# Optimization experiments

Measured on AMD Instinct MI355X. Metric: run time of the kernel, lower is better.

Reference implementation:

```python
import jax, jax.numpy as jnp
import numpy as np

INF = jnp.float32(1e30)


def _lsap_square(cost):
    """Exact Jonker-Volgenant shortest-augmenting-path LAP (port of scipy's
    rectangular_lsap) on a square [n, n] float32 cost matrix.
    Returns col4row[int32, n]: column assigned to each row (a permutation)."""
    n = cost.shape[0]
    rows = jnp.arange(n, dtype=jnp.int32)

    def outer(cur_row, carry):
        u, v, col4row, row4col = carry

        def dij_cond(st):
            return st[6] < 0

        def dij_body(st):
            i, minVal, SR, SC, sp, path, sink = st
            SR = SR.at[i].set(True)
            # tentative shortest-path cost through row i to every column
            r = minVal + cost[i] - u[i] - v
            upd = (~SC) & (r < sp)
            path = jnp.where(upd, i, path)
            sp = jnp.where(upd, r, sp)
            masked = jnp.where(SC, INF, sp)
            j = jnp.argmin(masked).astype(jnp.int32)
            minVal = masked[j]
            SC = SC.at[j].set(True)
            nxt = row4col[j]
            sink = jnp.where(nxt < 0, j, jnp.int32(-1))
            i = jnp.where(nxt < 0, i, nxt)
            return (i, minVal, SR, SC, sp, path, sink)

        init = (cur_row.astype(jnp.int32), jnp.float32(0.0),
                jnp.zeros(n, bool), jnp.zeros(n, bool),
                jnp.full(n, INF, jnp.float32),
                jnp.full(n, -1, jnp.int32), jnp.int32(-1))
        _, minVal, SR, SC, sp, path, sink = jax.lax.while_loop(dij_cond, dij_body, init)

        # dual potential updates
        sp_c4r = sp[jnp.clip(col4row, 0, n - 1)]
        du = jnp.where(rows == cur_row, minVal, minVal - sp_c4r)
        u = u + jnp.where(SR, du, jnp.float32(0.0))
        v = v - jnp.where(SC, minVal - sp, jnp.float32(0.0))

        # augment along the alternating path ending at sink
        def aug_cond(st):
            return ~st[3]

        def aug_body(st):
            j, c4r, r4c, done = st
            i = path[j]
            r4c = r4c.at[j].set(i)
            jnew = c4r[i]
            c4r = c4r.at[i].set(j)
            done = (i == cur_row)
            return (jnew, c4r, r4c, done)

        _, col4row, row4col, _ = jax.lax.while_loop(
            aug_cond, aug_body, (sink, col4row, row4col, jnp.bool_(False)))
        return (u, v, col4row, row4col)

    z = jnp.zeros(n, jnp.float32)
    neg1 = jnp.full(n, -1, jnp.int32)
    _, _, col4row, _ = jax.lax.fori_loop(0, n, outer, (z, z, neg1, neg1))
    return col4row


def _match(costs, mask):
    # costs: [B, N, N] (dim1 = preds, dim2 = objects); mask: [B, N] prefix-valid objects
    B, N, _ = costs.shape
    cols = jnp.arange(N, dtype=jnp.int32)

    def one(cost_b, mask_b):
        # rows = objects, cols = preds (matches costs[k][:, :n].T in torch code);
        # invalid object rows get constant cost 0, which leaves the optimal
        # matching of valid rows unchanged.
        cmat = jnp.where(mask_b[:, None], cost_b.T, jnp.float32(0.0))
        col4row = _lsap_square(cmat)
        # columns consumed by valid rows
        used = jnp.zeros(N, bool).at[col4row].set(mask_b)
        # unused columns ascending first, then used columns ascending
        leftover = jnp.sort(cols + N * used.astype(jnp.int32)) % N
        n = jnp.sum(mask_b).astype(jnp.int32)
        pos = jnp.clip(cols - n, 0, N - 1)
        # valid rows: matched column; invalid rows: leftover preds in ascending order
        return jnp.where(mask_b, col4row, leftover[pos])

    return jax.vmap(one)(costs, mask)


def setup_inputs() -> dict:
    key = jax.random.key(0)
    k1, k2 = jax.random.split(key)
    B, N = 64, 256
    costs = jax.random.normal(k1, (B, N, N), dtype=jnp.float32)
    lengths = jax.random.randint(k2, (B,), N // 2, N + 1)
    object_valid_mask = jnp.arange(N)[None, :] < lengths[:, None]  # prefix-true mask
    return {"costs": costs, "object_valid_mask": object_valid_mask}


def reference(costs, object_valid_mask):
    return _match(costs.astype(jnp.float32), object_valid_mask)
```

## Files before the change

### kernel.cpp

```cpp
#include <hip/hip_runtime.h>

#define NN 256
#define INFV 1e30f

__device__ __forceinline__ int mask_fmt(const void* m) {
    int w0 = ((const int*)m)[0];
    if (w0 == 1) return 0;
    if (w0 == 0x3F800000) return 1;
    return 2;
}
__device__ __forceinline__ bool mask_at(const void* m, int fmt, int idx) {
    if (fmt == 0) return ((const int*)m)[idx] != 0;
    if (fmt == 1) return ((const float*)m)[idx] != 0.0f;
    return ((const unsigned char*)m)[idx] != 0;
}

__global__ void transpose_mask_kernel(const float* __restrict__ costs,
                                      const void* __restrict__ mask,
                                      float* __restrict__ ws) {
    __shared__ float tile[32][33];
    const int b  = blockIdx.z;
    const int i0 = blockIdx.x * 32;
    const int j0 = blockIdx.y * 32;
    const int tx = threadIdx.x;
    const int ty = threadIdx.y;
    const int fmt = mask_fmt(mask);
    const float* Cb = costs + (size_t)b * NN * NN;
    float* Wb = ws + (size_t)b * NN * NN;

    #pragma unroll
    for (int k = 0; k < 32; k += 8) {
        tile[ty + k][tx] = Cb[(size_t)(j0 + ty + k) * NN + (i0 + tx)];
    }
    __syncthreads();
    #pragma unroll
    for (int k = 0; k < 32; k += 8) {
        const int i = i0 + ty + k;
        const int j = j0 + tx;
        const bool mv = mask_at(mask, fmt, b * NN + i);
        Wb[(size_t)i * NN + j] = mv ? tile[tx][ty + k] : 0.0f;
    }
}

__device__ __forceinline__ int rl(int v, int lane) {
    return __builtin_amdgcn_readlane(v, lane);
}
__device__ __forceinline__ float rlf(float v, int lane) {
    return __int_as_float(__builtin_amdgcn_readlane(__float_as_int(v), lane));
}
__device__ __forceinline__ int read4i(const int a[4], int idx) {
    const int lane = idx >> 2;
    const int v0 = rl(a[0], lane), v1 = rl(a[1], lane);
    const int v2 = rl(a[2], lane), v3 = rl(a[3], lane);
    const int lo = (idx & 1) ? v1 : v0;
    const int hi = (idx & 1) ? v3 : v2;
    return (idx & 2) ? hi : lo;
}
__device__ __forceinline__ float read4f(const float a[4], int idx) {
    const int lane = idx >> 2;
    const int v0 = rl(__float_as_int(a[0]), lane), v1 = rl(__float_as_int(a[1]), lane);
    const int v2 = rl(__float_as_int(a[2]), lane), v3 = rl(__float_as_int(a[3]), lane);
    const int lo = (idx & 1) ? v1 : v0;
    const int hi = (idx & 1) ? v3 : v2;
    return __int_as_float((idx & 2) ? hi : lo);
}
__device__ __forceinline__ void write4i(int (&a)[4], int idx, int val, int lane) {
    if (lane == (idx >> 2)) {
        switch (idx & 3) {
            case 0: a[0] = val; break;
            case 1: a[1] = val; break;
            case 2: a[2] = val; break;
            default: a[3] = val; break;
        }
    }
}

template <int CTRL>
__device__ __forceinline__ float dpp_mov_f(float x) {
    return __int_as_float(__builtin_amdgcn_update_dpp(
        __float_as_int(x), __float_as_int(x), CTRL, 0xf, 0xf, false));
}
__device__ __forceinline__ float wave_min64(float x) {
    x = fminf(x, dpp_mov_f<0x111>(x));
    x = fminf(x, dpp_mov_f<0x112>(x));
    x = fminf(x, dpp_mov_f<0x114>(x));
    x = fminf(x, dpp_mov_f<0x118>(x));
    x = fminf(x, dpp_mov_f<0x142>(x));
    x = fminf(x, dpp_mov_f<0x143>(x));
    return rlf(x, 63);
}

template <bool USE_WS>
__global__ __launch_bounds__(64)
void lap_kernel(const float* __restrict__ costs,
                const void* __restrict__ mask,
                const float* __restrict__ cmat,
                int* __restrict__ out,
                int rcache) {
    extern __shared__ float ldsrows[];

    const int b    = blockIdx.x;
    const int lane = threadIdx.x;

    __shared__ float sp_s[NN];
    __shared__ int   tmp_s[NN];

    const int fmt = mask_fmt(mask);

    int nloc = 0;
    #pragma unroll
    for (int r = 0; r < 4; ++r)
        nloc += mask_at(mask, fmt, b * NN + lane * 4 + r) ? 1 : 0;
    #pragma unroll
    for (int off = 32; off; off >>= 1) nloc += __shfl_xor(nloc, off);
    const int n = nloc;

    float u[4]  = {0.f, 0.f, 0.f, 0.f};
    float v[4]  = {0.f, 0.f, 0.f, 0.f};
    int  c4r[4] = {-1, -1, -1, -1};
    int  r4c[4] = {-1, -1, -1, -1};

    const float* CM = cmat + (size_t)b * NN * NN;
    const float* CB = costs + (size_t)b * NN * NN;

    if (USE_WS) {
        #pragma unroll 4
        for (int row = 0; row < rcache; ++row) {
            const int base = row * NN + lane * 4;
            *reinterpret_cast<float4*>(&ldsrows[base]) =
                *reinterpret_cast<const float4*>(CM + base);
        }
        __syncthreads();
    }

    for (int cur = 0; cur < NN; ++cur) {
        float sp[4]  = {INFV, INFV, INFV, INFV};
        int  path[4] = {-1, -1, -1, -1};
        int   SCm = 0, SRm = 0;
        int   i      = cur;
        float minVal = 0.0f;
        int   sink   = -1;

        for (int guard = 0; guard <= NN && sink < 0; ++guard) {
            if (lane == (i >> 2)) SRm |= 1 << (i & 3);

            float cc[4];
            if (USE_WS) {
                if (i < rcache) {
                    const float4 c4 = *reinterpret_cast<const float4*>(&ldsrows[i * NN + lane * 4]);
                    cc[0] = c4.x; cc[1] = c4.y; cc[2] = c4.z; cc[3] = c4.w;
                } else {
                    const float4 c4 = *reinterpret_cast<const float4*>(CM + (size_t)i * NN + lane * 4);
                    cc[0] = c4.x; cc[1] = c4.y; cc[2] = c4.z; cc[3] = c4.w;
                }
            } else {
                if (i < n) {
                    #pragma unroll
                    for (int r = 0; r < 4; ++r)
                        cc[r] = CB[(size_t)(lane * 4 + r) * NN + i];
                } else {
                    #pragma unroll
                    for (int r = 0; r < 4; ++r) cc[r] = 0.0f;
                }
            }
            const float u_i = read4f(u, i);

            float m[4];
            #pragma unroll
            for (int r = 0; r < 4; ++r) {
                const float rr = minVal + cc[r] - u_i - v[r];
                const bool sc = (SCm >> r) & 1;
                if (!sc && rr < sp[r]) { sp[r] = rr; path[r] = i; }
                m[r] = sc ? INFV : sp[r];
            }

            minVal = wave_min64(fminf(fminf(m[0], m[1]), fminf(m[2], m[3])));

            int cand = 4;
            if (m[3] == minVal) cand = 3;
            if (m[2] == minVal) cand = 2;
            if (m[1] == minVal) cand = 1;
            if (m[0] == minVal) cand = 0;
            const unsigned long long bal = __ballot(cand < 4);
            const int fl = (bal == 0ull) ? 0 : (__ffsll((long long)bal) - 1);
            const int j  = (bal == 0ull) ? 0 : (fl * 4 + rl(cand, fl));

            if (lane == (j >> 2)) SCm |= 1 << (j & 3);
            const int nxt = read4i(r4c, j);
            if (nxt < 0) sink = j;
            else         i = nxt;
        }

        *reinterpret_cast<float4*>(&sp_s[lane * 4]) = make_float4(sp[0], sp[1], sp[2], sp[3]);
        __syncthreads();

        #pragma unroll
        for (int r = 0; r < 4; ++r) {
            const int row = lane * 4 + r;
            if ((SRm >> r) & 1) {
                float du;
                if (row == cur) {
                    du = minVal;
                } else {
                    int c = c4r[r];
                    c = c < 0 ? 0 : c;
                    du = minVal - sp_s[c];
                }
                u[r] = u[r] + du;
            }
            if ((SCm >> r) & 1) v[r] = v[r] - (minVal - sp[r]);
        }
        __syncthreads();

        {
            int j = sink;
            for (int guard = 0; guard < NN; ++guard) {
                const int ii = read4i(path, j);
                write4i(r4c, j, ii, lane);
                const int jn = read4i(c4r, ii);
                write4i(c4r, ii, j, lane);
                if (ii == cur) break;
                j = jn;
            }
        }
    }

    int* ob = out + b * NN;
    #pragma unroll
    for (int r = 0; r < 4; ++r) {
        const int row = lane * 4 + r;
        if (row < n) ob[row] = c4r[r];
        tmp_s[lane * 4 + r] = r4c[r];
    }
    __syncthreads();
    if (lane == 0) {
        int cnt = 0;
        for (int c = 0; c < NN; ++c) {
            if (tmp_s[c] >= n) {
                ob[n + cnt] = c;
                ++cnt;
            }
        }
    }
}

extern "C" void kernel_launch(void* const* d_in, const int* in_sizes, int n_in,
                              void* d_out, int out_size, void* d_ws, size_t ws_size,
                              hipStream_t stream) {
    const float* costs = (const float*)d_in[0];
    const void*  mask  = d_in[1];
    int*         out   = (int*)d_out;

    const int B = in_sizes[1] / NN;
    const size_t need = (size_t)B * NN * NN * sizeof(float);

    if (ws_size >= need && d_ws != nullptr) {
        float* ws = (float*)d_ws;
        transpose_mask_kernel<<<dim3(NN / 32, NN / 32, B), dim3(32, 8), 0, stream>>>(costs, mask, ws);

        int rcache = 158;
        hipError_t e = hipFuncSetAttribute(
            reinterpret_cast<const void*>(&lap_kernel<true>),
            hipFuncAttributeMaxDynamicSharedMemorySize,
            rcache * NN * (int)sizeof(float));
        if (e != hipSuccess) rcache = 60;
        const size_t dynbytes = (size_t)rcache * NN * sizeof(float);

        lap_kernel<true><<<dim3(B), dim3(64), dynbytes, stream>>>(costs, mask, ws, out, rcache);
    } else {
        lap_kernel<false><<<dim3(B), dim3(64), 0, stream>>>(costs, mask, nullptr, out, 0);
    }
}
```

Before: 5.676 ms.

## Precompute masked-min off critical path and prefetch next cost row in Dijkstra loop

Restructures the inner Dijkstra step so the wave-wide minimum over previously masked columns (Vprev) is computed after selecting j, and the current step only reduces the freshly computed row costs before combining with Vprev. Scanned columns are masked by adding INF through a scadd array instead of branching on the SC bitmask. The next row load is issued right after j is known, so its latency can overlap the trailing reduction. This adds a second wave reduction per iteration and relies on INF arithmetic to keep masked columns from winning, and changes ballot logic which must match tie-breaking exactly.

```diff
diff --git a/kernel.cpp b/kernel.cpp
--- a/kernel.cpp
+++ b/kernel.cpp
@@ -123,6 +123,27 @@
     const float* CM = cmat + (size_t)b * NN * NN;
     const float* CB = costs + (size_t)b * NN * NN;
 
+    auto load_row = [&](int irow, float (&cc)[4]) {
+        if (USE_WS) {
+            if (irow < rcache) {
+                const float4 c4 = *reinterpret_cast<const float4*>(&ldsrows[irow * NN + lane * 4]);
+                cc[0] = c4.x; cc[1] = c4.y; cc[2] = c4.z; cc[3] = c4.w;
+            } else {
+                const float4 c4 = *reinterpret_cast<const float4*>(CM + (size_t)irow * NN + lane * 4);
+                cc[0] = c4.x; cc[1] = c4.y; cc[2] = c4.z; cc[3] = c4.w;
+            }
+        } else {
+            if (irow < n) {
+                #pragma unroll
+                for (int r = 0; r < 4; ++r)
+                    cc[r] = CB[(size_t)(lane * 4 + r) * NN + irow];
+            } else {
+                #pragma unroll
+                for (int r = 0; r < 4; ++r) cc[r] = 0.0f;
+            }
+        }
+    };
+
     if (USE_WS) {
         #pragma unroll 4
         for (int row = 0; row < rcache; ++row) {
@@ -134,61 +155,66 @@
     }
 
     for (int cur = 0; cur < NN; ++cur) {
-        float sp[4]  = {INFV, INFV, INFV, INFV};
-        int  path[4] = {-1, -1, -1, -1};
+        float sp[4]    = {INFV, INFV, INFV, INFV};
+        float mreg[4]  = {INFV, INFV, INFV, INFV};
+        float scadd[4] = {0.f, 0.f, 0.f, 0.f};
+        int  path[4]   = {-1, -1, -1, -1};
         int   SCm = 0, SRm = 0;
         int   i      = cur;
         float minVal = 0.0f;
+        float Vprev  = INFV;
         int   sink   = -1;
+
+        float cc[4];
+        load_row(i, cc);
 
         for (int guard = 0; guard <= NN && sink < 0; ++guard) {
             if (lane == (i >> 2)) SRm |= 1 << (i & 3);
-
-            float cc[4];
-            if (USE_WS) {
-                if (i < rcache) {
-                    const float4 c4 = *reinterpret_cast<const float4*>(&ldsrows[i * NN + lane * 4]);
-                    cc[0] = c4.x; cc[1] = c4.y; cc[2] = c4.z; cc[3] = c4.w;
-                } else {
-                    const float4 c4 = *reinterpret_cast<const float4*>(CM + (size_t)i * NN + lane * 4);
-                    cc[0] = c4.x; cc[1] = c4.y; cc[2] = c4.z; cc[3] = c4.w;
-                }
-            } else {
-                if (i < n) {
-                    #pragma unroll
-                    for (int r = 0; r < 4; ++r)
-                        cc[r] = CB[(size_t)(lane * 4 + r) * NN + i];
-                } else {
-                    #pragma unroll
-                    for (int r = 0; r < 4; ++r) cc[r] = 0.0f;
-                }
-            }
             const float u_i = read4f(u, i);
 
-            float m[4];
+            float rrm[4], m[4];
             #pragma unroll
             for (int r = 0; r < 4; ++r) {
                 const float rr = minVal + cc[r] - u_i - v[r];
-                const bool sc = (SCm >> r) & 1;
-                if (!sc && rr < sp[r]) { sp[r] = rr; path[r] = i; }
-                m[r] = sc ? INFV : sp[r];
-            }
-
-            minVal = wave_min64(fminf(fminf(m[0], m[1]), fminf(m[2], m[3])));
-
+                rrm[r] = rr + scadd[r];
+            }
+            minVal = fminf(wave_min64(fminf(fminf(rrm[0], rrm[1]), fminf(rrm[2], rrm[3]))),
+                           Vprev);
+
+            #pragma unroll
+            for (int r = 0; r < 4; ++r) {
+                const bool upd = rrm[r] < sp[r];
+                path[r] = upd ? i : path[r];
+                sp[r]   = fminf(sp[r], rrm[r]);
+                m[r]    = fminf(mreg[r], rrm[r]);
+            }
+
+            const float lanem = fminf(fminf(m[0], m[1]), fminf(m[2], m[3]));
+            const unsigned long long bal = __ballot(lanem == minVal);
             int cand = 4;
             if (m[3] == minVal) cand = 3;
             if (m[2] == minVal) cand = 2;
             if (m[1] == minVal) cand = 1;
             if (m[0] == minVal) cand = 0;
-            const unsigned long long bal = __ballot(cand < 4);
             const int fl = (bal == 0ull) ? 0 : (__ffsll((long long)bal) - 1);
             const int j  = (bal == 0ull) ? 0 : (fl * 4 + rl(cand, fl));
 
             if (lane == (j >> 2)) SCm |= 1 << (j & 3);
+            #pragma unroll
+            for (int r = 0; r < 4; ++r) {
+                const bool isj = (lane * 4 + r) == j;
+                mreg[r]  = isj ? INFV : m[r];
+                scadd[r] = isj ? INFV : scadd[r];
+            }
+
             const int nxt = read4i(r4c, j);
-            if (nxt < 0) sink = j;
-            else         i = nxt;
+            if (nxt < 0) {
+                sink = j;
+            } else {
+                i = nxt;
+                load_row(i, cc);
+            }
+            Vprev = wave_min64(fminf(fminf(mreg[0], mreg[1]), fminf(mreg[2], mreg[3])));
         }
 
         *reinterpret_cast<float4*>(&sp_s[lane * 4]) = make_float4(sp[0], sp[1], sp[2], sp[3]);
```

Measured after the change: 7.188 ms. 26.6% more time.
